# Performance work log

Hardware: AMD Instinct MI355X
Metric: run time of the kernel (lower is better)

The kernel has to match this reference:

```python
import jax, jax.numpy as jnp
import numpy as np

V, D, H = 5000, 300, 256
B, T = 16, 512


def setup_inputs() -> dict:
    key = jax.random.key(0)
    ks = jax.random.split(key, 14)
    def w(k, shape):
        return jax.random.normal(k, shape, dtype=jnp.float32) * 0.02
    return {
        "x": jax.random.normal(ks[0], (B, T, V), dtype=jnp.float32),
        "hidden_state": jax.random.normal(ks[1], (1, H), dtype=jnp.float32),
        "context_state": jax.random.normal(ks[2], (1, H), dtype=jnp.float32),
        "E": w(ks[3], (D, V)),      # embedding Linear weight [out,in]
        "Wf": w(ks[4], (H, D)), "Uf": w(ks[5], (H, H)),
        "Wg": w(ks[6], (H, D)), "Ug": w(ks[7], (H, H)),
        "Wi": w(ks[8], (H, D)), "Ui": w(ks[9], (H, H)),
        "Wo": w(ks[10], (H, D)), "Uo": w(ks[11], (H, H)),
        "Wout": w(ks[12], (V, H)),
    }


def reference(x, hidden_state, context_state, E, Wf, Uf, Wg, Ug, Wi, Ui, Wo, Uo, Wout):
    # Precompute all input-side projections in one batched pass: [B,T,D]
    emb = jnp.einsum('btv,dv->btd', x, E)
    # Stack input-gate GEMMs: [B,T,4H]
    Wx = jnp.concatenate([Wf, Wg, Wi, Wo], axis=0)  # [4H, D]
    gates_x = jnp.einsum('btd,gd->btg', emb, Wx)    # [B, T, 4H]
    Uh = jnp.concatenate([Uf, Ug, Ui, Uo], axis=0)  # [4H, H]

    h0 = jnp.broadcast_to(hidden_state, (x.shape[0], hidden_state.shape[-1]))
    c0 = jnp.broadcast_to(context_state, (x.shape[0], context_state.shape[-1]))

    Hn = hidden_state.shape[-1]

    def step(carry, gx):
        h, c = carry
        gh = h @ Uh.T                     # [B, 4H]
        z = gx + gh
        f = jax.nn.sigmoid(z[:, 0*Hn:1*Hn])
        g = jnp.tanh(z[:, 1*Hn:2*Hn])
        i = jax.nn.sigmoid(z[:, 2*Hn:3*Hn])
        o = jax.nn.sigmoid(z[:, 3*Hn:4*Hn])
        c_new = g * i + c * f
        h_new = o * jnp.tanh(c_new)
        # NOTE: faithful to source - output projects g, not h
        out = g @ Wout.T                  # [B, V]
        return (h_new, c_new), out

    _, outs = jax.lax.scan(step, (h0, c0), jnp.swapaxes(gates_x, 0, 1))
    return jnp.swapaxes(outs, 0, 1)       # [B, T, V]
```

## Files before the change

kernel.cpp:

```cpp
#include <hip/hip_runtime.h>
#include <stdint.h>

typedef unsigned short u16;
typedef unsigned int u32;
typedef __attribute__((ext_vector_type(8))) __bf16 bf16x8;
typedef __attribute__((ext_vector_type(4))) float f32x4;
typedef __attribute__((ext_vector_type(4))) u32 u32x4;
typedef __attribute__((ext_vector_type(2))) u32 u32x2;
typedef __attribute__((ext_vector_type(4))) int i32x4;

#define DEV __device__ __forceinline__

constexpr int V = 5000, D = 300, H = 256, BB = 16, T = 512;
constexpr int M = BB * T;
constexpr int DP = 320;
constexpr int KP = 5024;
constexpr int G4 = 1024;
constexpr int NPAD = 5120;

constexpr size_t OFF_EB    = 0;
constexpr size_t OFF_WXB   = OFF_EB    + (size_t)DP * KP * 2;
constexpr size_t OFF_UHB   = OFF_WXB   + (size_t)G4 * DP * 2;
constexpr size_t OFF_WOUTB = OFF_UHB   + (size_t)G4 * H * 2;
constexpr size_t OFF_GATES = OFF_WOUTB + (size_t)NPAD * H * 2;
constexpr size_t OFF_GALL  = OFF_GATES + (size_t)T * BB * G4 * 2;
constexpr size_t OFF_EMB   = OFF_GALL  + (size_t)M * H * 2;

DEV u16 f2bf(float f) {
  u32 i = __builtin_bit_cast(u32, f);
  return (u16)((i + 0x7FFFu + ((i >> 16) & 1u)) >> 16);
}
DEV float bf2f(u16 u) { return __builtin_bit_cast(float, (u32)u << 16); }
DEV f32x4 MFMA(u32x4 a, u32x4 b, f32x4 c) {
  return __builtin_amdgcn_mfma_f32_16x16x32_bf16(
      __builtin_bit_cast(bf16x8, a), __builtin_bit_cast(bf16x8, b), c, 0, 0, 0);
}
DEV i32x4 MFMA8(u32x4 a, u32x4 b, i32x4 c) {
  return __builtin_amdgcn_mfma_i32_16x16x64_i8(
      __builtin_bit_cast(i32x4, a), __builtin_bit_cast(i32x4, b), c, 0, 0, 0);
}
DEV float sigm(float x) { return 1.f / (1.f + __expf(-x)); }
DEV float tanh_s(float x) { float e = __expf(2.f * x); return 1.f - 2.f / (e + 1.f); }

DEV void bar_lds() {
  asm volatile("s_waitcnt lgkmcnt(0)" ::: "memory");
  __builtin_amdgcn_sched_barrier(0);
  __builtin_amdgcn_s_barrier();
  __builtin_amdgcn_sched_barrier(0);
}

__global__ __launch_bounds__(256) void k_prep(
    const float* __restrict__ E, const float* __restrict__ Wf, const float* __restrict__ Wg,
    const float* __restrict__ Wi, const float* __restrict__ Wo,
    const float* __restrict__ Wout, char* __restrict__ ws) {
  u16* Eb = (u16*)(ws + OFF_EB);
  u16* Wxb = (u16*)(ws + OFF_WXB);
  u16* Wob = (u16*)(ws + OFF_WOUTB);

  const int NE = DP * KP, NW = G4 * DP, NWO = NPAD * H;
  const int total = NE + NW + NWO;
  for (int i = blockIdx.x * blockDim.x + threadIdx.x; i < total; i += gridDim.x * blockDim.x) {
    int j = i;
    if (j < NE) {
      int nn = j / KP, k = j % KP;
      Eb[j] = f2bf((nn < D && k < V) ? E[(size_t)nn * V + k] : 0.f);
      continue;
    }
    j -= NE;
    if (j < NW) {
      int r = j / DP, k = j % DP;
      const float* Wp = (r < 256) ? Wf : (r < 512) ? Wg : (r < 768) ? Wi : Wo;
      Wxb[j] = f2bf((k < D) ? Wp[(size_t)(r & 255) * D + k] : 0.f);
      continue;
    }
    j -= NW;
    if (j < NWO) {
      int nn = j / H, k = j % H;
      Wob[j] = f2bf((nn < V) ? Wout[(size_t)nn * H + k] : 0.f);
      continue;
    }
  }
}

__global__ __launch_bounds__(256) void k_prep_u(
    const float* __restrict__ Uf, const float* __restrict__ Ug,
    const float* __restrict__ Ui, const float* __restrict__ Uo, char* __restrict__ ws) {
  char* qU = ws + OFF_UHB;
  float* zsc = (float*)(ws + OFF_UHB + (size_t)G4 * H);
  const int row = blockIdx.x * 4 + (threadIdx.x >> 6);
  const int lane = threadIdx.x & 63;
  const float* Up = (row < 256) ? Uf : (row < 512) ? Ug : (row < 768) ? Ui : Uo;
  f32x4 v = *(const f32x4*)(Up + (size_t)(row & 255) * H + lane * 4);
  float m = fmaxf(fmaxf(fabsf(v[0]), fabsf(v[1])), fmaxf(fabsf(v[2]), fabsf(v[3])));
  for (int i = 1; i < 64; i <<= 1) m = fmaxf(m, __shfl_xor(m, i));
  float inv = (m > 0.f) ? 127.f / m : 0.f;
  int q0 = (int)rintf(v[0] * inv), q1 = (int)rintf(v[1] * inv);
  int q2 = (int)rintf(v[2] * inv), q3 = (int)rintf(v[3] * inv);
  q0 = max(-127, min(127, q0)); q1 = max(-127, min(127, q1));
  q2 = max(-127, min(127, q2)); q3 = max(-127, min(127, q3));
  u32 pk = (u32)(q0 & 255) | ((u32)(q1 & 255) << 8) | ((u32)(q2 & 255) << 16) |
           ((u32)(q3 & 255) << 24);
  *(u32*)(qU + (size_t)row * H + lane * 4) = pk;
  if (lane == 0) zsc[row] = m / 16129.f;
}

__global__ __launch_bounds__(256) void k_emb(const float* __restrict__ x, char* __restrict__ ws) {
  const u16* Eb = (const u16*)(ws + OFF_EB);
  float* emb = (float*)(ws + OFF_EMB);
  __shared__ __align__(16) u16 As[32 * 40];
  __shared__ __align__(16) u16 Bs[320 * 40];

  const int tid = threadIdx.x;
  const int m0 = blockIdx.x * 32;
  const int lane = tid & 63, wv = tid >> 6;
  const int l15 = lane & 15, lc = lane >> 4;
  const int mt = wv & 1, ntb = (wv >> 1) * 10;

  f32x4 acc[10];
#pragma unroll
  for (int j = 0; j < 10; j++) acc[j] = (f32x4){0.f, 0.f, 0.f, 0.f};

  const int ar = tid >> 3, ak = (tid & 7) * 4;

  f32x4 xv0, xv1;
  u32x4 ev0[5], ev1[5];

#define EMB_ISSUE(SFX, KS)                                                        \
  do {                                                                            \
    int k0_ = (KS) * 32;                                                          \
    {                                                                             \
      size_t base_ = (size_t)(m0 + ar) * V + k0_ + ak;                            \
      if (k0_ + ak + 3 < V) {                                                     \
        xv##SFX = *(const f32x4*)(x + base_);                                     \
      } else {                                                                    \
        f32x4 t_;                                                                 \
        t_[0] = (k0_ + ak + 0 < V) ? x[base_ + 0] : 0.f;                          \
        t_[1] = (k0_ + ak + 1 < V) ? x[base_ + 1] : 0.f;                          \
        t_[2] = (k0_ + ak + 2 < V) ? x[base_ + 2] : 0.f;                          \
        t_[3] = (k0_ + ak + 3 < V) ? x[base_ + 3] : 0.f;                          \
        xv##SFX = t_;                                                             \
      }                                                                           \
    }                                                                             \
    _Pragma("unroll") for (int j_ = 0; j_ < 5; j_++) {                            \
      int cc_ = tid + 256 * j_;                                                   \
      int n_ = cc_ >> 2, ko_ = (cc_ & 3) * 8;                                     \
      ev##SFX[j_] = *(const u32x4*)(Eb + (size_t)n_ * KP + k0_ + ko_);            \
    }                                                                             \
  } while (0)

#define EMB_WRITE(SFX)                                                            \
  do {                                                                            \
    union { u16 u[4]; u32x2 v; } ua_;                                             \
    ua_.u[0] = f2bf(xv##SFX[0]); ua_.u[1] = f2bf(xv##SFX[1]);                     \
    ua_.u[2] = f2bf(xv##SFX[2]); ua_.u[3] = f2bf(xv##SFX[3]);                     \
    *(u32x2*)&As[ar * 40 + ak] = ua_.v;                                           \
    _Pragma("unroll") for (int j_ = 0; j_ < 5; j_++) {                            \
      int cc_ = tid + 256 * j_;                                                   \
      int n_ = cc_ >> 2, ko_ = (cc_ & 3) * 8;                                     \
      *(u32x4*)&Bs[n_ * 40 + ko_] = ev##SFX[j_];                                  \
    }                                                                             \
  } while (0)

  auto emb_compute = [&]() {
    u32x4 a = *(const u32x4*)&As[(mt * 16 + l15) * 40 + lc * 8];
#pragma unroll
    for (int j = 0; j < 10; j++) {
      u32x4 b = *(const u32x4*)&Bs[((ntb + j) * 16 + l15) * 40 + lc * 8];
      acc[j] = MFMA(a, b, acc[j]);
    }
  };

  constexpr int NK = 157;
  EMB_ISSUE(0, 0);
  EMB_ISSUE(1, 1);
  for (int ks = 0; ks < NK; ks += 2) {
    __syncthreads();
    EMB_WRITE(0);
    if (ks + 2 < NK) EMB_ISSUE(0, ks + 2);
    __syncthreads();
    emb_compute();
    if (ks + 1 < NK) {
      __syncthreads();
      EMB_WRITE(1);
      if (ks + 3 < NK) EMB_ISSUE(1, ks + 3);
      __syncthreads();
      emb_compute();
    }
  }
#pragma unroll
  for (int j = 0; j < 10; j++) {
    int nn = (ntb + j) * 16 + l15;
    int mrow = m0 + mt * 16 + lc * 4;
#pragma unroll
    for (int r = 0; r < 4; r++) emb[(size_t)(mrow + r) * DP + nn] = acc[j][r];
  }
#undef EMB_ISSUE
#undef EMB_WRITE
}

__global__ __launch_bounds__(256) void k_gates(char* __restrict__ ws) {
  const float* emb = (const float*)(ws + OFF_EMB);
  const u16* Wxb = (const u16*)(ws + OFF_WXB);
  u16* gates = (u16*)(ws + OFF_GATES);
  __shared__ __align__(16) u16 As[64 * 40];
  __shared__ __align__(16) u16 Bs[256 * 40];

  const int tid = threadIdx.x;
  const int blk = blockIdx.x;
  const int m0 = (blk >> 2) * 64, n0 = (blk & 3) * 256;
  const int lane = tid & 63, wv = tid >> 6;
  const int l15 = lane & 15, lc = lane >> 4;

  f32x4 acc[16];
#pragma unroll
  for (int j = 0; j < 16; j++) acc[j] = (f32x4){0.f, 0.f, 0.f, 0.f};

  f32x4 av0[2], av1[2];
  u32x4 bv0[4], bv1[4];

#define GT_ISSUE(SFX, KS)                                                         \
  do {                                                                            \
    int k0_ = (KS) * 32;                                                          \
    _Pragma("unroll") for (int j_ = 0; j_ < 2; j_++) {                            \
      int c_ = tid + 256 * j_;                                                    \
      int r_ = c_ >> 3, ko_ = (c_ & 7) * 4;                                       \
      av##SFX[j_] = *(const f32x4*)(emb + (size_t)(m0 + r_) * DP + k0_ + ko_);    \
    }                                                                             \
    _Pragma("unroll") for (int j_ = 0; j_ < 4; j_++) {                            \
      int c_ = tid + 256 * j_;                                                    \
      int n_ = c_ >> 2, ko_ = (c_ & 3) * 8;                                       \
      bv##SFX[j_] = *(const u32x4*)(Wxb + (size_t)(n0 + n_) * DP + k0_ + ko_);    \
    }                                                                             \
  } while (0)

#define GT_WRITE(SFX)                                                             \
  do {                                                                            \
    _Pragma("unroll") for (int j_ = 0; j_ < 2; j_++) {                            \
      int c_ = tid + 256 * j_;                                                    \
      int r_ = c_ >> 3, ko_ = (c_ & 7) * 4;                                       \
      union { u16 u[4]; u32x2 v; } ua_;                                           \
      ua_.u[0] = f2bf(av##SFX[j_][0]); ua_.u[1] = f2bf(av##SFX[j_][1]);           \
      ua_.u[2] = f2bf(av##SFX[j_][2]); ua_.u[3] = f2bf(av##SFX[j_][3]);           \
      *(u32x2*)&As[r_ * 40 + ko_] = ua_.v;                                        \
    }                                                                             \
    _Pragma("unroll") for (int j_ = 0; j_ < 4; j_++) {                            \
      int c_ = tid + 256 * j_;                                                    \
      int n_ = c_ >> 2, ko_ = (c_ & 3) * 8;                                       \
      *(u32x4*)&Bs[n_ * 40 + ko_] = bv##SFX[j_];                                  \
    }                                                                             \
  } while (0)

  auto gt_compute = [&]() {
    u32x4 a = *(const u32x4*)&As[(wv * 16 + l15) * 40 + lc * 8];
#pragma unroll
    for (int nt = 0; nt < 16; nt++) {
      u32x4 b = *(const u32x4*)&Bs[(nt * 16 + l15) * 40 + lc * 8];
      acc[nt] = MFMA(a, b, acc[nt]);
    }
  };

  constexpr int NK = 10;
  GT_ISSUE(0, 0);
  GT_ISSUE(1, 1);
  for (int ks = 0; ks < NK; ks += 2) {
    __syncthreads();
    GT_WRITE(0);
    if (ks + 2 < NK) GT_ISSUE(0, ks + 2);
    __syncthreads();
    gt_compute();
    __syncthreads();
    GT_WRITE(1);
    if (ks + 3 < NK) GT_ISSUE(1, ks + 3);
    __syncthreads();
    gt_compute();
  }
#pragma unroll
  for (int nt = 0; nt < 16; nt++) {
#pragma unroll
    for (int r = 0; r < 4; r++) {
      int m = m0 + wv * 16 + lc * 4 + r;
      int col = n0 + nt * 16 + l15;
      int q = col >> 8, nn = col & 255;
      gates[(((size_t)(m & (T - 1)) * 16 + (m >> 9)) * 256 + nn) * 4 + q] = f2bf(acc[nt][r]);
    }
  }
#undef GT_ISSUE
#undef GT_WRITE
}

__global__ __launch_bounds__(512) void k_scan(const float* __restrict__ hidden,
                                              const float* __restrict__ ctx,
                                              char* __restrict__ ws) {
  const char* qU = (const char*)(ws + OFF_UHB);
  const float* zsc = (const float*)(ws + OFF_UHB + (size_t)G4 * H);
  const u16* gates = (const u16*)(ws + OFF_GATES);
  u16* gall = (u16*)(ws + OFF_GALL);

  __shared__ __align__(16) char pq[2][2][256];
  __shared__ __align__(16) int zl2[2][1040];

  const int tid = threadIdx.x;
  const int lane = tid & 63, wv = tid >> 6;
  const int l15 = lane & 15, lc = lane >> 4;

  u32x4 uq[8][4];
#pragma unroll
  for (int i = 0; i < 8; i++)
#pragma unroll
    for (int kt = 0; kt < 4; kt++) {
      int row = (wv * 8 + i) * 16 + l15;
      uq[i][kt] = *(const u32x4*)(qU + (size_t)row * H + kt * 64 + lc * 16);
    }

  const int b = tid >> 8, n = tid & 255;
  const int b_glob = blockIdx.x * 2 + b;
  float c = ctx[n];
  const float zs0 = zsc[n], zs1 = zsc[n + 256], zs2 = zsc[n + 512], zs3 = zsc[n + 768];
  u32x2 gxc = *(const u32x2*)(gates + (((size_t)0 * 16 + b_glob) * 256 + n) * 4);
  u32x2 gxn = *(const u32x2*)(gates + (((size_t)1 * 16 + b_glob) * 256 + n) * 4);

  {
    float h0 = hidden[n];
    h0 = fminf(3.999f, fmaxf(-3.999f, h0));
    pq[0][b][n] = (char)(int)rintf(h0 * 31.75f);
  }
  __syncthreads();

#pragma unroll 1
  for (int t = 0; t < T; ++t) {
    const int par = t & 1;
    u32x4 bfr[4];
#pragma unroll
    for (int kt = 0; kt < 4; kt++)
      bfr[kt] = *(const u32x4*)&pq[par][l15 & 1][kt * 64 + lc * 16];

#pragma unroll
    for (int i = 0; i < 8; i++) {
      i32x4 acc = {0, 0, 0, 0};
#pragma unroll
      for (int kt = 0; kt < 4; kt++) acc = MFMA8(uq[i][kt], bfr[kt], acc);
      if (l15 < 2) *(i32x4*)&zl2[l15][(wv * 8 + i) * 16 + lc * 4] = acc;
    }
    bar_lds();

    const float hs = (t == 0) ? 4.f : 1.f;
    float z0 = (float)zl2[b][n] * zs0 * hs + bf2f((u16)(gxc[0] & 0xFFFFu));
    float z1 = (float)zl2[b][n + 256] * zs1 * hs + bf2f((u16)(gxc[0] >> 16));
    float z2 = (float)zl2[b][n + 512] * zs2 * hs + bf2f((u16)(gxc[1] & 0xFFFFu));
    float z3 = (float)zl2[b][n + 768] * zs3 * hs + bf2f((u16)(gxc[1] >> 16));
    float fv = sigm(z0), gv = tanh_s(z1), iv = sigm(z2), ov = sigm(z3);
    c = gv * iv + c * fv;
    float hn = ov * tanh_s(c);
    gall[((size_t)b_glob * T + t) * H + n] = f2bf(gv);
    pq[par ^ 1][b][n] = (char)(int)rintf(hn * 127.f);
    gxc = gxn;
    int t2 = (t + 2 < T) ? (t + 2) : t;
    gxn = *(const u32x2*)(gates + (((size_t)t2 * 16 + b_glob) * 256 + n) * 4);
    bar_lds();
  }
}

__global__ __launch_bounds__(256) void k_out(char* __restrict__ ws, float* __restrict__ out) {
  const u16* gall = (const u16*)(ws + OFF_GALL);
  const u16* Wob = (const u16*)(ws + OFF_WOUTB);
  __shared__ __align__(16) u16 As[64 * 40];
  __shared__ __align__(16) u16 Bs[256 * 40];

  const int tid = threadIdx.x;
  const int blk = blockIdx.x;
  const int m0 = (blk / 20) * 64, n0 = (blk % 20) * 256;
  const int lane = tid & 63, wv = tid >> 6;
  const int l15 = lane & 15, lc = lane >> 4;

  f32x4 acc[16];
#pragma unroll
  for (int j = 0; j < 16; j++) acc[j] = (f32x4){0.f, 0.f, 0.f, 0.f};

  u32x4 av0, av1;
  u32x4 bv0[4], bv1[4];

#define OUT_ISSUE(SFX, KS)                                                        \
  do {                                                                            \
    int k0_ = (KS) * 32;                                                          \
    {                                                                             \
      int r_ = tid >> 2, ko_ = (tid & 3) * 8;                                     \
      av##SFX = *(const u32x4*)(gall + (size_t)(m0 + r_) * H + k0_ + ko_);        \
    }                                                                             \
    _Pragma("unroll") for (int j_ = 0; j_ < 4; j_++) {                            \
      int c_ = tid + 256 * j_;                                                    \
      int n_ = c_ >> 2, ko_ = (c_ & 3) * 8;                                       \
      bv##SFX[j_] = *(const u32x4*)(Wob + (size_t)(n0 + n_) * H + k0_ + ko_);     \
    }                                                                             \
  } while (0)

#define OUT_WRITE(SFX)                                                            \
  do {                                                                            \
    {                                                                             \
      int r_ = tid >> 2, ko_ = (tid & 3) * 8;                                     \
      *(u32x4*)&As[r_ * 40 + ko_] = av##SFX;                                      \
    }                                                                             \
    _Pragma("unroll") for (int j_ = 0; j_ < 4; j_++) {                            \
      int c_ = tid + 256 * j_;                                                    \
      int n_ = c_ >> 2, ko_ = (c_ & 3) * 8;                                       \
      *(u32x4*)&Bs[n_ * 40 + ko_] = bv##SFX[j_];                                  \
    }                                                                             \
  } while (0)

  auto out_compute = [&]() {
    u32x4 a = *(const u32x4*)&As[(wv * 16 + l15) * 40 + lc * 8];
#pragma unroll
    for (int nt = 0; nt < 16; nt++) {
      u32x4 b = *(const u32x4*)&Bs[(nt * 16 + l15) * 40 + lc * 8];
      acc[nt] = MFMA(a, b, acc[nt]);
    }
  };

  constexpr int NK = 8;
  OUT_ISSUE(0, 0);
  OUT_ISSUE(1, 1);
  for (int ks = 0; ks < NK; ks += 2) {
    __syncthreads();
    OUT_WRITE(0);
    if (ks + 2 < NK) OUT_ISSUE(0, ks + 2);
    __syncthreads();
    out_compute();
    __syncthreads();
    OUT_WRITE(1);
    if (ks + 3 < NK) OUT_ISSUE(1, ks + 3);
    __syncthreads();
    out_compute();
  }
#pragma unroll
  for (int nt = 0; nt < 16; nt++) {
    int vcol = n0 + nt * 16 + l15;
    if (vcol < V) {
#pragma unroll
      for (int r = 0; r < 4; r++) {
        int m = m0 + wv * 16 + lc * 4 + r;
        out[(size_t)m * V + vcol] = acc[nt][r];
      }
    }
  }
#undef OUT_ISSUE
#undef OUT_WRITE
}

extern "C" void kernel_launch(void* const* d_in, const int* in_sizes, int n_in,
                              void* d_out, int out_size, void* d_ws, size_t ws_size,
                              hipStream_t stream) {
  (void)in_sizes; (void)n_in; (void)out_size; (void)ws_size;
  const float* x      = (const float*)d_in[0];
  const float* hidden = (const float*)d_in[1];
  const float* ctx    = (const float*)d_in[2];
  const float* E      = (const float*)d_in[3];
  const float* Wf     = (const float*)d_in[4];
  const float* Uf     = (const float*)d_in[5];
  const float* Wg     = (const float*)d_in[6];
  const float* Ug     = (const float*)d_in[7];
  const float* Wi     = (const float*)d_in[8];
  const float* Ui     = (const float*)d_in[9];
  const float* Wo     = (const float*)d_in[10];
  const float* Uo     = (const float*)d_in[11];
  const float* Wout   = (const float*)d_in[12];
  char* ws = (char*)d_ws;
  float* out = (float*)d_out;

  hipLaunchKernelGGL(k_prep, dim3(1024), dim3(256), 0, stream,
                     E, Wf, Wg, Wi, Wo, Wout, ws);
  hipLaunchKernelGGL(k_prep_u, dim3(256), dim3(256), 0, stream, Uf, Ug, Ui, Uo, ws);
  hipLaunchKernelGGL(k_emb, dim3(M / 32), dim3(256), 0, stream, x, ws);
  hipLaunchKernelGGL(k_gates, dim3((M / 64) * 4), dim3(256), 0, stream, ws);
  hipLaunchKernelGGL(k_scan, dim3(8), dim3(512), 0, stream, hidden, ctx, ws);
  hipLaunchKernelGGL(k_out, dim3((M / 64) * 20), dim3(256), 0, stream, ws, out);
}
```

Before: 817.1 us.

## Repartition scan gate rows per wave to drop intra-step block barrier

Each wave now owns all four gate rows (f,g,i,o) for its own 32 hidden units, so the gate pre-activations it needs come from its own MFMAs. The cross-wave exchange through LDS and the block-wide barrier between the recurrent matmul and the elementwise update are replaced by a per-wave LDS write followed by a wait on lgkmcnt. The LDS scratch is double-buffered by step parity so the next step's writes cannot overwrite values still being read. This shortens the per-timestep critical path of the serial recurrence. The risk is correctness if LDS visibility within a wave is not ordered as assumed, and a different lane-to-unit mapping for the gate loads.

```diff
diff --git a/kernel.cpp b/kernel.cpp
--- a/kernel.cpp
+++ b/kernel.cpp
@@ -297,22 +297,25 @@
   u16* gall = (u16*)(ws + OFF_GALL);
 
   __shared__ __align__(16) char pq[2][2][256];
-  __shared__ __align__(16) int zl2[2][1040];
+  __shared__ __align__(16) int zw[2][8][8][2][16];
 
   const int tid = threadIdx.x;
   const int lane = tid & 63, wv = tid >> 6;
   const int l15 = lane & 15, lc = lane >> 4;
 
-  u32x4 uq[8][4];
-#pragma unroll
-  for (int i = 0; i < 8; i++)
-#pragma unroll
-    for (int kt = 0; kt < 4; kt++) {
-      int row = (wv * 8 + i) * 16 + l15;
-      uq[i][kt] = *(const u32x4*)(qU + (size_t)row * H + kt * 64 + lc * 16);
-    }
-
-  const int b = tid >> 8, n = tid & 255;
+  u32x4 uq[4][2][4];
+#pragma unroll
+  for (int gg = 0; gg < 4; gg++)
+#pragma unroll
+    for (int j = 0; j < 2; j++)
+#pragma unroll
+      for (int kt = 0; kt < 4; kt++)
+        uq[gg][j][kt] = *(const u32x4*)(
+            qU + (size_t)(gg * 256 + wv * 32 + j * 16 + l15) * H + kt * 64 + lc * 16);
+
+  const int b = lane >> 5, np = lane & 31;
+  const int n = wv * 32 + np;
+  const int jj = (np >> 4) & 1, rr = np & 15;
   const int b_glob = blockIdx.x * 2 + b;
   float c = ctx[n];
   const float zs0 = zsc[n], zs1 = zsc[n + 256], zs2 = zsc[n + 512], zs3 = zsc[n + 768];
@@ -320,9 +323,10 @@
   u32x2 gxn = *(const u32x2*)(gates + (((size_t)1 * 16 + b_glob) * 256 + n) * 4);
 
   {
-    float h0 = hidden[n];
+    const int b0 = tid >> 8, n0i = tid & 255;
+    float h0 = hidden[n0i];
     h0 = fminf(3.999f, fmaxf(-3.999f, h0));
-    pq[0][b][n] = (char)(int)rintf(h0 * 31.75f);
+    pq[0][b0][n0i] = (char)(int)rintf(h0 * 31.75f);
   }
   __syncthreads();
 
@@ -334,20 +338,31 @@
     for (int kt = 0; kt < 4; kt++)
       bfr[kt] = *(const u32x4*)&pq[par][l15 & 1][kt * 64 + lc * 16];
 
-#pragma unroll
-    for (int i = 0; i < 8; i++) {
-      i32x4 acc = {0, 0, 0, 0};
-#pragma unroll
-      for (int kt = 0; kt < 4; kt++) acc = MFMA8(uq[i][kt], bfr[kt], acc);
-      if (l15 < 2) *(i32x4*)&zl2[l15][(wv * 8 + i) * 16 + lc * 4] = acc;
-    }
-    bar_lds();
+    i32x4 acc[4][2];
+#pragma unroll
+    for (int gg = 0; gg < 4; gg++)
+#pragma unroll
+      for (int j = 0; j < 2; j++) {
+        i32x4 a = {0, 0, 0, 0};
+#pragma unroll
+        for (int kt = 0; kt < 4; kt++) a = MFMA8(uq[gg][j][kt], bfr[kt], a);
+        acc[gg][j] = a;
+      }
+    if (l15 < 2) {
+#pragma unroll
+      for (int gg = 0; gg < 4; gg++)
+#pragma unroll
+        for (int j = 0; j < 2; j++)
+          *(i32x4*)&zw[par][wv][gg * 2 + j][l15][lc * 4] = acc[gg][j];
+    }
+    asm volatile("s_waitcnt lgkmcnt(0)" ::: "memory");
+    __builtin_amdgcn_sched_barrier(0);
 
     const float hs = (t == 0) ? 4.f : 1.f;
-    float z0 = (float)zl2[b][n] * zs0 * hs + bf2f((u16)(gxc[0] & 0xFFFFu));
-    float z1 = (float)zl2[b][n + 256] * zs1 * hs + bf2f((u16)(gxc[0] >> 16));
-    float z2 = (float)zl2[b][n + 512] * zs2 * hs + bf2f((u16)(gxc[1] & 0xFFFFu));
-    float z3 = (float)zl2[b][n + 768] * zs3 * hs + bf2f((u16)(gxc[1] >> 16));
+    float z0 = (float)zw[par][wv][0 + jj][b][rr] * (zs0 * hs) + bf2f((u16)(gxc[0] & 0xFFFFu));
+    float z1 = (float)zw[par][wv][2 + jj][b][rr] * (zs1 * hs) + bf2f((u16)(gxc[0] >> 16));
+    float z2 = (float)zw[par][wv][4 + jj][b][rr] * (zs2 * hs) + bf2f((u16)(gxc[1] & 0xFFFFu));
+    float z3 = (float)zw[par][wv][6 + jj][b][rr] * (zs3 * hs) + bf2f((u16)(gxc[1] >> 16));
     float fv = sigm(z0), gv = tanh_s(z1), iv = sigm(z2), ov = sigm(z3);
     c = gv * iv + c * fv;
     float hn = ov * tanh_s(c);
```

New measurement: 822.8 us. About the same (+0.7%).
